# Kernel tuning notes

Measured on AMD Instinct MI355X. Metric: run time of the kernel, lower is better.

The kernel has to match this reference:

```python
import jax, jax.numpy as jnp
import numpy as np


def setup_inputs() -> dict:
    key = jax.random.key(0)
    k0, k1, k2, k3, k4, k5 = jax.random.split(key, 6)
    L1, L2, B, D = 512, 512, 32, 1024
    inputs1 = jax.random.normal(k0, (L1, B, D), dtype=jnp.float32)
    inputs2 = jax.random.normal(k1, (L2, B, D), dtype=jnp.float32)
    # mask value 0 marks a valid token (module keeps pairs where both masks == 0)
    mask1 = jax.random.randint(k2, (L1, B), 0, 2, dtype=jnp.int64)
    mask2 = jax.random.randint(k3, (L2, B), 0, 2, dtype=jnp.int64)
    W = jax.random.normal(k4, (D, D), dtype=jnp.float32) * 0.02
    b = jax.random.normal(k5, (1,), dtype=jnp.float32) * 0.02
    return {"inputs1": inputs1, "inputs2": inputs2, "mask1": mask1,
            "mask2": mask2, "W": W, "b": b, "k": 256}


def reference(inputs1, inputs2, mask1, mask2, W, b, k):
    # inputs: [len, bsz, hdim]; masks: [len, bsz]
    H1 = jnp.transpose(inputs1, (1, 0, 2))  # [B, L1, D]
    H2 = jnp.transpose(inputs2, (1, 0, 2))  # [B, L2, D]
    # bilinear scores: H1 @ W @ H2^T + b, then relu  -> [B, L1, L2]
    S = jax.nn.relu(jnp.einsum('bid,de,bje->bij', H1, W, H2) + b[0])
    # pair is valid iff both mask entries are 0
    valid = (mask1.T[:, :, None] == 0) & (mask2.T[:, None, :] == 0)  # [B, L1, L2]
    B = S.shape[0]
    S_flat = jnp.where(valid.reshape(B, -1), S.reshape(B, -1), -jnp.inf)
    num_elems = S_flat.shape[1]
    k_actual = min(k, num_elems)
    q, _ = jax.lax.top_k(S_flat, k_actual)  # [B, k_actual]
    # replace -inf tail entries with the last finite value in each row
    neg = jnp.isneginf(q)
    q_num_finite = k_actual - neg.sum(axis=-1)  # [B]
    fill = jnp.take_along_axis(q, (q_num_finite - 1)[:, None], axis=1)  # [B, 1]
    q = jnp.where(neg, fill, q)
    if k_actual < k:
        q = jnp.concatenate(
            [q, jnp.broadcast_to(q[:, -1:], (B, k - k_actual))], axis=1)
    return q
```

## Files before the change

kernel.cpp:

```cpp
#include <hip/hip_runtime.h>

typedef __bf16 bf16_t;
typedef bf16_t bf16x8 __attribute__((ext_vector_type(8)));
typedef float floatx4 __attribute__((ext_vector_type(4)));

#define L1C 512
#define L2C 512
#define BC  32
#define DC  1024
#define KTOP 256
#define NBIN 4096
#define CAP  512
#define NT   64
#define FBUF 16384

__device__ __forceinline__ unsigned short f2bf(float f) {
    unsigned u = __float_as_uint(f);
    u += 0x7FFFu + ((u >> 16) & 1u);
    return (unsigned short)(u >> 16);
}

__device__ __forceinline__ void g2l16(const unsigned short* g, unsigned short* l) {
    __builtin_amdgcn_global_load_lds((const unsigned int*)g, (unsigned int*)l,
                                     16, 0, 0);
}

__device__ __forceinline__ float decode_key(unsigned k) {
    return __uint_as_float(k & 0x7FFFFFFFu);
}

__global__ __launch_bounds__(512) void scan_kernel(
    const int* __restrict__ mask1, const int* __restrict__ mask2,
    int* __restrict__ idx1, int* __restrict__ idx2,
    unsigned* __restrict__ nv1, unsigned* __restrict__ nv2,
    unsigned* __restrict__ cnt) {
    __shared__ unsigned sc[512];
    int b = blockIdx.x, t = threadIdx.x;
    for (int which = 0; which < 2; which++) {
        const int* m = which ? mask2 : mask1;
        int* idx = which ? idx2 : idx1;
        unsigned v = (m[t * BC + b] == 0) ? 1u : 0u;
        sc[t] = v;
        __syncthreads();
        for (int off = 1; off < 512; off <<= 1) {
            unsigned x = (t >= off) ? sc[t - off] : 0u;
            __syncthreads();
            sc[t] += x;
            __syncthreads();
        }
        if (v) idx[b * 512 + sc[t] - 1] = t;
        if (t == 511) { if (which) nv2[b] = sc[511]; else nv1[b] = sc[511]; }
        __syncthreads();
    }
    if (t < NT) cnt[b * NT + t] = 0;
}

__global__ __launch_bounds__(256) void prep_kernel(
    const float* __restrict__ in1, const float* __restrict__ in2,
    const float* __restrict__ W,
    const int* __restrict__ idx1, const int* __restrict__ idx2,
    const unsigned* __restrict__ nv1, const unsigned* __restrict__ nv2,
    unsigned short* __restrict__ A1c, unsigned short* __restrict__ A2c,
    unsigned short* __restrict__ Wb) {
    int r = blockIdx.x, t = threadIdx.x;
    const float* src;
    unsigned short* dst;
    if (r < 2 * 16384) {
        int which = r >> 14;
        int rr = r & 16383;
        int b = rr >> 9, vi = rr & 511;
        unsigned nv = which ? nv2[b] : nv1[b];
        unsigned pad = (nv + 63u) & ~63u;
        if ((unsigned)vi >= pad) return;
        dst = (which ? A2c : A1c) + ((size_t)b * 512 + vi) * DC;
        if ((unsigned)vi < nv) {
            int l = (which ? idx2 : idx1)[b * 512 + vi];
            src = (which ? in2 : in1) + (size_t)(l * BC + b) * DC;
        } else {
            ushort4 z = {0, 0, 0, 0};
            reinterpret_cast<ushort4*>(dst)[t] = z;
            return;
        }
    } else {
        int r3 = r - 2 * 16384;
        src = W + (size_t)r3 * DC;
        dst = Wb + (size_t)r3 * DC;
    }
    float4 v = reinterpret_cast<const float4*>(src)[t];
    ushort4 o;
    o.x = f2bf(v.x); o.y = f2bf(v.y); o.z = f2bf(v.z); o.w = f2bf(v.w);
    reinterpret_cast<ushort4*>(dst)[t] = o;
}

__global__ __launch_bounds__(256) void gemm1_kernel(
    const unsigned short* __restrict__ A,
    const unsigned short* __restrict__ Bt,
    unsigned short* __restrict__ C,
    const unsigned* __restrict__ nv2) {
    int bi = blockIdx.x >> 2, mt = blockIdx.x & 3;
    unsigned pad2 = (nv2[bi] + 63u) & ~63u;
    if ((unsigned)(mt * 128) >= pad2) return;
    __shared__ unsigned short As[2][128][32];
    __shared__ unsigned short Bs[2][128][32];
    int tid = threadIdx.x;
    int wave = tid >> 6, lane = tid & 63;
    int lane15 = lane & 15, quad = lane >> 4;
    int wm = wave >> 1, wn = wave & 1;
    size_t m0 = (size_t)bi * 512 + mt * 128;
    size_t n0 = (size_t)blockIdx.y * 128;

    floatx4 zero = {0.f, 0.f, 0.f, 0.f};
    floatx4 acc[4][4];
#pragma unroll
    for (int i = 0; i < 4; i++)
#pragma unroll
        for (int j = 0; j < 4; j++) acc[i][j] = zero;

    for (int k0 = 0; k0 < DC; k0 += 64) {
#pragma unroll
        for (int c = 0; c < 4; c++) {
            int cid = c * 256 + tid;
            int h = cid >> 9, row = (cid >> 2) & 127, col8 = (cid & 3) * 8;
            unsigned short* lb = &As[0][0][0] + (c * 256 + wave * 64) * 8;
            g2l16(&A[(m0 + row) * DC + k0 + h * 32 + col8], lb);
            unsigned short* lb2 = &Bs[0][0][0] + (c * 256 + wave * 64) * 8;
            g2l16(&Bt[(n0 + row) * DC + k0 + h * 32 + col8], lb2);
        }
        __syncthreads();
#pragma unroll
        for (int h = 0; h < 2; h++) {
            bf16x8 af[4], bfr[4];
#pragma unroll
            for (int mi = 0; mi < 4; mi++)
                af[mi] = *reinterpret_cast<const bf16x8*>(
                    &As[h][wm * 64 + mi * 16 + lane15][quad * 8]);
#pragma unroll
            for (int ni = 0; ni < 4; ni++)
                bfr[ni] = *reinterpret_cast<const bf16x8*>(
                    &Bs[h][wn * 64 + ni * 16 + lane15][quad * 8]);
#pragma unroll
            for (int mi = 0; mi < 4; mi++)
#pragma unroll
                for (int ni = 0; ni < 4; ni++)
                    acc[mi][ni] = __builtin_amdgcn_mfma_f32_16x16x32_bf16(
                        af[mi], bfr[ni], acc[mi][ni], 0, 0, 0);
        }
        __syncthreads();
    }
#pragma unroll
    for (int mi = 0; mi < 4; mi++)
#pragma unroll
        for (int ni = 0; ni < 4; ni++)
#pragma unroll
            for (int r = 0; r < 4; r++) {
                size_t row = m0 + wm * 64 + mi * 16 + quad * 4 + r;
                size_t col = n0 + wn * 64 + ni * 16 + lane15;
                C[row * DC + col] = f2bf(acc[mi][ni][r]);
            }
}

__global__ __launch_bounds__(256) void gemm2_kernel(
    const unsigned short* __restrict__ A1c,
    const unsigned short* __restrict__ V,
    const unsigned* __restrict__ nv1, const unsigned* __restrict__ nv2,
    const float* __restrict__ bptr,
    unsigned* __restrict__ cand,
    unsigned* __restrict__ cnt) {
    int L = blockIdx.x;
    int xcd = L & 7, tile = (L >> 3) & 63, chunk = L >> 9;
    int b = xcd + (chunk << 3);
    int tx = tile & 7, ty = tile >> 3;
    int m0 = ty * 64, n0 = tx * 64;
    int gblk = b * NT + tile;
    int tid = threadIdx.x;
    unsigned nv1v = nv1[b], nv2v = nv2[b];
    unsigned pad1 = (nv1v + 63u) & ~63u, pad2 = (nv2v + 63u) & ~63u;
    if ((unsigned)m0 >= pad1 || (unsigned)n0 >= pad2) {
        if (tid == 0) cnt[gblk] = 0;
        return;
    }
    __shared__ unsigned short As[2][64][32];
    __shared__ unsigned short Bs[2][64][32];
    __shared__ unsigned lh[NBIN];
    __shared__ unsigned csum[256];
    __shared__ unsigned sel_c, sel_a, tsh, lcnt, zeq;
    int wave = tid >> 6, lane = tid & 63;
    int lane15 = lane & 15, quad = lane >> 4;
    const unsigned short* Ab = A1c + (size_t)b * 512 * DC;
    const unsigned short* Bb = V + (size_t)b * 512 * DC;

    for (int i = tid; i < NBIN; i += 256) lh[i] = 0;
    if (tid == 0) { sel_c = 0xFFFFFFFFu; lcnt = 0; zeq = 0; }

    floatx4 zero = {0.f, 0.f, 0.f, 0.f};
    floatx4 acc[4];
#pragma unroll
    for (int i = 0; i < 4; i++) acc[i] = zero;

    for (int k0 = 0; k0 < DC; k0 += 64) {
#pragma unroll
        for (int c = 0; c < 2; c++) {
            int cid = c * 256 + tid;
            int h = cid >> 8, row = (cid >> 2) & 63, col8 = (cid & 3) * 8;
            unsigned short* lb = &As[0][0][0] + (c * 256 + wave * 64) * 8;
            g2l16(&Ab[(size_t)(m0 + row) * DC + k0 + h * 32 + col8], lb);
            unsigned short* lb2 = &Bs[0][0][0] + (c * 256 + wave * 64) * 8;
            g2l16(&Bb[(size_t)(n0 + row) * DC + k0 + h * 32 + col8], lb2);
        }
        __syncthreads();
#pragma unroll
        for (int h = 0; h < 2; h++) {
            bf16x8 af, bfr[4];
            af = *reinterpret_cast<const bf16x8*>(
                &As[h][wave * 16 + lane15][quad * 8]);
#pragma unroll
            for (int ni = 0; ni < 4; ni++)
                bfr[ni] = *reinterpret_cast<const bf16x8*>(
                    &Bs[h][ni * 16 + lane15][quad * 8]);
#pragma unroll
            for (int ni = 0; ni < 4; ni++)
                acc[ni] = __builtin_amdgcn_mfma_f32_16x16x32_bf16(
                    af, bfr[ni], acc[ni], 0, 0, 0);
        }
        __syncthreads();
    }

    float bias = bptr[0];
    unsigned zc = 0;
#pragma unroll
    for (int ni = 0; ni < 4; ni++) {
        int jl = n0 + ni * 16 + lane15;
        int v2 = (unsigned)jl < nv2v;
#pragma unroll
        for (int r = 0; r < 4; r++) {
            int il = m0 + wave * 16 + quad * 4 + r;
            float s = acc[ni][r] + bias;
            if (v2 && (unsigned)il < nv1v) {
                if (s > 0.f)
                    atomicAdd(&lh[(__float_as_uint(s) | 0x80000000u) >> 20], 1u);
                else
                    zc++;
            }
        }
    }
    if (zc) atomicAdd(&lh[2048], zc);
    __syncthreads();
    unsigned s16 = 0;
#pragma unroll
    for (int i = 0; i < 16; i++) s16 += lh[tid * 16 + i];
    csum[tid] = s16;
    __syncthreads();
    for (int off = 1; off < 256; off <<= 1) {
        unsigned v = (tid + off < 256) ? csum[tid + off] : 0u;
        __syncthreads();
        csum[tid] += v;
        __syncthreads();
    }
    {
        unsigned above = (tid < 255) ? csum[tid + 1] : 0u;
        if (tid >= 128 && csum[tid] >= KTOP && above < KTOP) {
            sel_c = (unsigned)tid; sel_a = above;
        }
    }
    __syncthreads();
    if (tid == 0) {
        if (sel_c == 0xFFFFFFFFu) {
            tsh = 2048u << 20;
        } else {
            unsigned cum = sel_a, bin = 2048;
            for (int bb = (int)sel_c * 16 + 15; bb >= (int)sel_c * 16; --bb) {
                unsigned hb = lh[bb];
                if (cum + hb >= KTOP) { bin = (unsigned)bb; break; }
                cum += hb;
            }
            tsh = bin << 20;
        }
    }
    __syncthreads();
    unsigned T = tsh;
    unsigned base = (unsigned)gblk * CAP;
#pragma unroll
    for (int ni = 0; ni < 4; ni++) {
        int jl = n0 + ni * 16 + lane15;
        int v2 = (unsigned)jl < nv2v;
#pragma unroll
        for (int r = 0; r < 4; r++) {
            int il = m0 + wave * 16 + quad * 4 + r;
            float s = acc[ni][r] + bias;
            s = s > 0.f ? s : 0.f;
            unsigned key = (v2 && (unsigned)il < nv1v)
                               ? (__float_as_uint(s) | 0x80000000u) : 0u;
            if (key > T) {
                unsigned p = atomicAdd(&lcnt, 1u);
                if (p < CAP) cand[base + p] = key;
            } else if (key == T) {
                unsigned z = atomicAdd(&zeq, 1u);
                if (z < KTOP) {
                    unsigned p = atomicAdd(&lcnt, 1u);
                    if (p < CAP) cand[base + p] = key;
                }
            }
        }
    }
    __syncthreads();
    if (tid == 0) cnt[gblk] = lcnt < CAP ? lcnt : CAP;
}

__global__ __launch_bounds__(1024) void final_kernel(
    const unsigned* __restrict__ cand, const unsigned* __restrict__ cnt,
    float* __restrict__ out) {
    __shared__ unsigned buf[FBUF];
    __shared__ unsigned h[NBIN];
    __shared__ unsigned ss[256];
    __shared__ unsigned scnt_s[NT], off_s[NT];
    __shared__ unsigned ntot_s, sel_c, sel_a, B_s, R_s, mcount;
    __shared__ int have_s;
    __shared__ unsigned srt[256];
    int b = blockIdx.x, tid = threadIdx.x;
    int wv = tid >> 6, ln = tid & 63;

    if (tid < NT) {
        unsigned c = cnt[b * NT + tid];
        scnt_s[tid] = c < CAP ? c : CAP;
    }
    __syncthreads();
    if (tid == 0) {
        unsigned o = 0;
        for (int i = 0; i < NT; i++) {
            unsigned c = scnt_s[i];
            if (o + c > FBUF) c = (o < FBUF) ? FBUF - o : 0;
            scnt_s[i] = c;
            off_s[i] = o;
            o += c;
        }
        ntot_s = o;
        have_s = 1;
    }
    __syncthreads();
    for (int s = wv; s < NT; s += 16) {
        unsigned c = scnt_s[s], o = off_s[s];
        const unsigned* p = cand + (size_t)(b * NT + s) * CAP;
        for (unsigned i = ln; i < c; i += 64) buf[o + i] = p[i];
    }
    __syncthreads();
    unsigned n = ntot_s;

    unsigned Kr = KTOP;
    unsigned pfx = 0;
    unsigned kth = 0;
    for (int pass = 0; pass < 3; pass++) {
        int bins = (pass < 2) ? NBIN : 256;
        int shift = (pass == 0) ? 20 : (pass == 1) ? 8 : 0;
        int nch = bins >> 4;
        for (int i = tid; i < bins; i += 1024) h[i] = 0;
        __syncthreads();
        for (unsigned i = tid; i < n; i += 1024) {
            unsigned k = buf[i];
            bool ok = (pass == 0) ||
                      (pass == 1 && (k >> 20) == pfx) ||
                      (pass == 2 && (k >> 8) == pfx);
            if (ok) atomicAdd(&h[(k >> shift) & (bins - 1)], 1u);
        }
        __syncthreads();
        if (tid < nch) {
            unsigned s = 0;
#pragma unroll
            for (int i = 0; i < 16; i++) s += h[tid * 16 + i];
            ss[tid] = s;
        }
        __syncthreads();
        for (int off = 1; off < nch; off <<= 1) {
            unsigned v = 0;
            if (tid < nch && tid + (unsigned)off < (unsigned)nch) v = ss[tid + off];
            __syncthreads();
            if (tid < nch) ss[tid] += v;
            __syncthreads();
        }
        if (pass == 0) {
            if (tid == 0) have_s = (ss[0] >= KTOP);
            __syncthreads();
            if (!have_s) break;
        }
        if (tid < nch) {
            unsigned above = (tid + 1 < (unsigned)nch) ? ss[tid + 1] : 0u;
            if (above < Kr && ss[tid] >= Kr) { sel_c = tid; sel_a = above; }
        }
        __syncthreads();
        if (tid == 0) {
            unsigned cum = sel_a;
            for (int bb = (int)sel_c * 16 + 15; bb >= (int)sel_c * 16; --bb) {
                unsigned hb = h[bb];
                if (cum + hb >= Kr) { B_s = (unsigned)bb; R_s = Kr - cum; break; }
                cum += hb;
            }
        }
        __syncthreads();
        unsigned Bv = B_s;
        Kr = R_s;
        if (pass == 0) pfx = Bv;
        else if (pass == 1) pfx = (pfx << 12) | Bv;
        else kth = (pfx << 8) | Bv;
        __syncthreads();
    }

    if (tid == 0) mcount = 0;
    __syncthreads();
    int have = have_s;
    unsigned lim = have ? kth : 0u;
    for (unsigned i = tid; i < n; i += 1024) {
        unsigned k = buf[i];
        if (k > lim) {
            unsigned p = atomicAdd(&mcount, 1u);
            if (p < 256) srt[p] = k;
        }
    }
    __syncthreads();
    unsigned m = mcount;
    if (tid < 256 && tid >= (int)m) srt[tid] = have ? kth : 0u;
    for (int k2 = 2; k2 <= 256; k2 <<= 1) {
        for (int j2 = k2 >> 1; j2 > 0; j2 >>= 1) {
            __syncthreads();
            if (tid < 256) {
                int ixj = tid ^ j2;
                if (ixj > tid) {
                    unsigned a = srt[tid], c = srt[ixj];
                    bool up = (tid & k2) == 0;
                    if (up ? (a < c) : (a > c)) { srt[tid] = c; srt[ixj] = a; }
                }
            }
        }
    }
    __syncthreads();
    if (tid < 256) {
        unsigned nval = have ? KTOP : (m < KTOP ? m : KTOP);
        float v;
        if ((unsigned)tid < nval) v = decode_key(srt[tid]);
        else v = (nval > 0) ? decode_key(srt[nval - 1]) : -__builtin_inff();
        out[b * KTOP + tid] = v;
    }
}

extern "C" void kernel_launch(void* const* d_in, const int* in_sizes, int n_in,
                              void* d_out, int out_size, void* d_ws, size_t ws_size,
                              hipStream_t stream) {
    const float* in1   = (const float*)d_in[0];
    const float* in2   = (const float*)d_in[1];
    const int*   mask1 = (const int*)d_in[2];
    const int*   mask2 = (const int*)d_in[3];
    const float* W     = (const float*)d_in[4];
    const float* bias  = (const float*)d_in[5];
    float* out = (float*)d_out;

    char* ws = (char*)d_ws;
    size_t off = 0;
    const size_t nElem = (size_t)512 * BC * DC;
    unsigned short* A1c = (unsigned short*)(ws + off); off += nElem * 2;
    unsigned short* A2c = (unsigned short*)(ws + off); off += nElem * 2;
    unsigned short* Wb  = (unsigned short*)(ws + off); off += (size_t)DC * DC * 2;
    unsigned short* V   = (unsigned short*)(ws + off); off += nElem * 2;
    unsigned* cand = (unsigned*)(ws + off); off += (size_t)BC * NT * CAP * 4;
    unsigned* cnt  = (unsigned*)(ws + off); off += (size_t)BC * NT * 4;
    int* idx1 = (int*)(ws + off); off += (size_t)BC * 512 * 4;
    int* idx2 = (int*)(ws + off); off += (size_t)BC * 512 * 4;
    unsigned* nv1 = (unsigned*)(ws + off); off += BC * 4;
    unsigned* nv2 = (unsigned*)(ws + off); off += BC * 4;

    scan_kernel<<<BC, 512, 0, stream>>>(mask1, mask2, idx1, idx2, nv1, nv2, cnt);
    prep_kernel<<<2 * 16384 + 1024, 256, 0, stream>>>(
        in1, in2, W, idx1, idx2, nv1, nv2, A1c, A2c, Wb);
    gemm1_kernel<<<dim3(128, 8), 256, 0, stream>>>(A2c, Wb, V, nv2);
    gemm2_kernel<<<2048, 256, 0, stream>>>(A1c, V, nv1, nv2, bias, cand, cnt);
    final_kernel<<<BC, 1024, 0, stream>>>(cand, cnt, out);
}
```

Baseline: 248.2 us.

## Double-buffer LDS tiles in both GEMMs and shrink gemm1 M-tile

Both GEMM kernels now keep two LDS buffers. The loads for the next 64-wide K slice are issued before the MFMA work on the current slice, so global-to-LDS transfer can overlap compute instead of waiting behind a barrier. gemm1 also changes its block tile from 128x128 to 64x128, with each wave owning a 64x32 strip, and launches twice as many blocks. That gives more parallelism and finer skipping of padded rows, at the cost of more redundant loads of the B operand. Double buffering doubles the GEMM LDS footprint, which may reduce occupancy, especially in gemm2, which also holds a 4096-bin histogram in LDS.

```diff
diff --git a/kernel.cpp b/kernel.cpp
--- a/kernel.cpp
+++ b/kernel.cpp
@@ -97,51 +97,62 @@
     const unsigned short* __restrict__ Bt,
     unsigned short* __restrict__ C,
     const unsigned* __restrict__ nv2) {
-    int bi = blockIdx.x >> 2, mt = blockIdx.x & 3;
+    int bi = blockIdx.x >> 3, mt = blockIdx.x & 7;
     unsigned pad2 = (nv2[bi] + 63u) & ~63u;
-    if ((unsigned)(mt * 128) >= pad2) return;
-    __shared__ unsigned short As[2][128][32];
-    __shared__ unsigned short Bs[2][128][32];
+    if ((unsigned)(mt * 64) >= pad2) return;
+    __shared__ unsigned short As[2][2][64][32];
+    __shared__ unsigned short Bs[2][2][128][32];
     int tid = threadIdx.x;
     int wave = tid >> 6, lane = tid & 63;
     int lane15 = lane & 15, quad = lane >> 4;
-    int wm = wave >> 1, wn = wave & 1;
-    size_t m0 = (size_t)bi * 512 + mt * 128;
+    size_t m0 = (size_t)bi * 512 + mt * 64;
     size_t n0 = (size_t)blockIdx.y * 128;
 
     floatx4 zero = {0.f, 0.f, 0.f, 0.f};
-    floatx4 acc[4][4];
+    floatx4 acc[4][2];
 #pragma unroll
     for (int i = 0; i < 4; i++)
 #pragma unroll
-        for (int j = 0; j < 4; j++) acc[i][j] = zero;
-
-    for (int k0 = 0; k0 < DC; k0 += 64) {
+        for (int j = 0; j < 2; j++) acc[i][j] = zero;
+
+    auto stage = [&](int sb, int k0) {
+#pragma unroll
+        for (int c = 0; c < 2; c++) {
+            int cid = c * 256 + tid;
+            int h = cid >> 8, row = (cid >> 2) & 63, col8 = (cid & 3) * 8;
+            unsigned short* lb = &As[sb][0][0][0] + (c * 256 + wave * 64) * 8;
+            g2l16(&A[(m0 + row) * DC + k0 + h * 32 + col8], lb);
+        }
 #pragma unroll
         for (int c = 0; c < 4; c++) {
             int cid = c * 256 + tid;
             int h = cid >> 9, row = (cid >> 2) & 127, col8 = (cid & 3) * 8;
-            unsigned short* lb = &As[0][0][0] + (c * 256 + wave * 64) * 8;
-            g2l16(&A[(m0 + row) * DC + k0 + h * 32 + col8], lb);
-            unsigned short* lb2 = &Bs[0][0][0] + (c * 256 + wave * 64) * 8;
-            g2l16(&Bt[(n0 + row) * DC + k0 + h * 32 + col8], lb2);
-        }
-        __syncthreads();
+            unsigned short* lb = &Bs[sb][0][0][0] + (c * 256 + wave * 64) * 8;
+            g2l16(&Bt[(n0 + row) * DC + k0 + h * 32 + col8], lb);
+        }
+    };
+
+    stage(0, 0);
+    __syncthreads();
+#pragma unroll
+    for (int t = 0; t < DC / 64; t++) {
+        int buf = t & 1;
+        if (t + 1 < DC / 64) stage(buf ^ 1, (t + 1) * 64);
 #pragma unroll
         for (int h = 0; h < 2; h++) {
-            bf16x8 af[4], bfr[4];
+            bf16x8 af[4], bfr[2];
 #pragma unroll
             for (int mi = 0; mi < 4; mi++)
                 af[mi] = *reinterpret_cast<const bf16x8*>(
-                    &As[h][wm * 64 + mi * 16 + lane15][quad * 8]);
-#pragma unroll
-            for (int ni = 0; ni < 4; ni++)
+                    &As[buf][h][mi * 16 + lane15][quad * 8]);
+#pragma unroll
+            for (int ni = 0; ni < 2; ni++)
                 bfr[ni] = *reinterpret_cast<const bf16x8*>(
-                    &Bs[h][wn * 64 + ni * 16 + lane15][quad * 8]);
+                    &Bs[buf][h][wave * 32 + ni * 16 + lane15][quad * 8]);
 #pragma unroll
             for (int mi = 0; mi < 4; mi++)
 #pragma unroll
-                for (int ni = 0; ni < 4; ni++)
+                for (int ni = 0; ni < 2; ni++)
                     acc[mi][ni] = __builtin_amdgcn_mfma_f32_16x16x32_bf16(
                         af[mi], bfr[ni], acc[mi][ni], 0, 0, 0);
         }
@@ -150,11 +161,11 @@
 #pragma unroll
     for (int mi = 0; mi < 4; mi++)
 #pragma unroll
-        for (int ni = 0; ni < 4; ni++)
+        for (int ni = 0; ni < 2; ni++)
 #pragma unroll
             for (int r = 0; r < 4; r++) {
-                size_t row = m0 + wm * 64 + mi * 16 + quad * 4 + r;
-                size_t col = n0 + wn * 64 + ni * 16 + lane15;
+                size_t row = m0 + mi * 16 + quad * 4 + r;
+                size_t col = n0 + wave * 32 + ni * 16 + lane15;
                 C[row * DC + col] = f2bf(acc[mi][ni][r]);
             }
 }
@@ -179,8 +190,8 @@
         if (tid == 0) cnt[gblk] = 0;
         return;
     }
-    __shared__ unsigned short As[2][64][32];
-    __shared__ unsigned short Bs[2][64][32];
+    __shared__ unsigned short As[2][2][64][32];
+    __shared__ unsigned short Bs[2][2][64][32];
     __shared__ unsigned lh[NBIN];
     __shared__ unsigned csum[256];
     __shared__ unsigned sel_c, sel_a, tsh, lcnt, zeq;
@@ -197,26 +208,33 @@
 #pragma unroll
     for (int i = 0; i < 4; i++) acc[i] = zero;
 
-    for (int k0 = 0; k0 < DC; k0 += 64) {
+    auto stage = [&](int sb, int k0) {
 #pragma unroll
         for (int c = 0; c < 2; c++) {
             int cid = c * 256 + tid;
             int h = cid >> 8, row = (cid >> 2) & 63, col8 = (cid & 3) * 8;
-            unsigned short* lb = &As[0][0][0] + (c * 256 + wave * 64) * 8;
+            unsigned short* lb = &As[sb][0][0][0] + (c * 256 + wave * 64) * 8;
             g2l16(&Ab[(size_t)(m0 + row) * DC + k0 + h * 32 + col8], lb);
-            unsigned short* lb2 = &Bs[0][0][0] + (c * 256 + wave * 64) * 8;
+            unsigned short* lb2 = &Bs[sb][0][0][0] + (c * 256 + wave * 64) * 8;
             g2l16(&Bb[(size_t)(n0 + row) * DC + k0 + h * 32 + col8], lb2);
         }
-        __syncthreads();
+    };
+
+    stage(0, 0);
+    __syncthreads();
+#pragma unroll
+    for (int t = 0; t < DC / 64; t++) {
+        int buf = t & 1;
+        if (t + 1 < DC / 64) stage(buf ^ 1, (t + 1) * 64);
 #pragma unroll
         for (int h = 0; h < 2; h++) {
             bf16x8 af, bfr[4];
             af = *reinterpret_cast<const bf16x8*>(
-                &As[h][wave * 16 + lane15][quad * 8]);
+                &As[buf][h][wave * 16 + lane15][quad * 8]);
 #pragma unroll
             for (int ni = 0; ni < 4; ni++)
                 bfr[ni] = *reinterpret_cast<const bf16x8*>(
-                    &Bs[h][ni * 16 + lane15][quad * 8]);
+                    &Bs[buf][h][ni * 16 + lane15][quad * 8]);
 #pragma unroll
             for (int ni = 0; ni < 4; ni++)
                 acc[ni] = __builtin_amdgcn_mfma_f32_16x16x32_bf16(
@@ -468,7 +486,7 @@
     scan_kernel<<<BC, 512, 0, stream>>>(mask1, mask2, idx1, idx2, nv1, nv2, cnt);
     prep_kernel<<<2 * 16384 + 1024, 256, 0, stream>>>(
         in1, in2, W, idx1, idx2, nv1, nv2, A1c, A2c, Wb);
-    gemm1_kernel<<<dim3(128, 8), 256, 0, stream>>>(A2c, Wb, V, nv2);
+    gemm1_kernel<<<dim3(256, 8), 256, 0, stream>>>(A2c, Wb, V, nv2);
     gemm2_kernel<<<2048, 256, 0, stream>>>(A1c, V, nv1, nv2, bias, cand, cnt);
     final_kernel<<<BC, 1024, 0, stream>>>(cand, cnt, out);
 }
```

Result: slower. 268.2 us (+8.1%).

## Double-buffer LDS tiles in both GEMM kernels with async prefetch of next k-step

Applied to the files above, without the earlier changes.

Both GEMM kernels now keep two LDS buffers and issue the global-to-LDS loads for the next k-step before computing on the current one. Partial s_waitcnt vmcnt counts replace the full __syncthreads, so the next tile's loads can stay in flight while the MFMAs run. The aim is to hide global memory latency behind compute. The cost is doubled LDS use, which may lower occupancy, especially in gemm2 where the histogram also lives in LDS. The correctness of the barriers now depends on hand-written waitcnt counts and compiler fences.

```diff
diff --git a/kernel.cpp b/kernel.cpp
--- a/kernel.cpp
+++ b/kernel.cpp
@@ -28,6 +28,8 @@
 __device__ __forceinline__ float decode_key(unsigned k) {
     return __uint_as_float(k & 0x7FFFFFFFu);
 }
+
+#define CFENCE asm volatile("" ::: "memory")
 
 __global__ __launch_bounds__(512) void scan_kernel(
     const int* __restrict__ mask1, const int* __restrict__ mask2,
@@ -100,8 +102,10 @@
     int bi = blockIdx.x >> 2, mt = blockIdx.x & 3;
     unsigned pad2 = (nv2[bi] + 63u) & ~63u;
     if ((unsigned)(mt * 128) >= pad2) return;
-    __shared__ unsigned short As[2][128][32];
-    __shared__ unsigned short Bs[2][128][32];
+    __shared__ unsigned short As0[2][128][32];
+    __shared__ unsigned short Bs0[2][128][32];
+    __shared__ unsigned short As1[2][128][32];
+    __shared__ unsigned short Bs1[2][128][32];
     int tid = threadIdx.x;
     int wave = tid >> 6, lane = tid & 63;
     int lane15 = lane & 15, quad = lane >> 4;
@@ -116,28 +120,49 @@
 #pragma unroll
         for (int j = 0; j < 4; j++) acc[i][j] = zero;
 
-    for (int k0 = 0; k0 < DC; k0 += 64) {
+    auto stage = [&](unsigned short* la, unsigned short* lb, int k0) {
 #pragma unroll
         for (int c = 0; c < 4; c++) {
             int cid = c * 256 + tid;
             int h = cid >> 9, row = (cid >> 2) & 127, col8 = (cid & 3) * 8;
-            unsigned short* lb = &As[0][0][0] + (c * 256 + wave * 64) * 8;
-            g2l16(&A[(m0 + row) * DC + k0 + h * 32 + col8], lb);
-            unsigned short* lb2 = &Bs[0][0][0] + (c * 256 + wave * 64) * 8;
-            g2l16(&Bt[(n0 + row) * DC + k0 + h * 32 + col8], lb2);
-        }
-        __syncthreads();
+            g2l16(&A[(m0 + row) * DC + k0 + h * 32 + col8],
+                  la + (c * 256 + wave * 64) * 8);
+        }
+#pragma unroll
+        for (int c = 0; c < 4; c++) {
+            int cid = c * 256 + tid;
+            int h = cid >> 9, row = (cid >> 2) & 127, col8 = (cid & 3) * 8;
+            g2l16(&Bt[(n0 + row) * DC + k0 + h * 32 + col8],
+                  lb + (c * 256 + wave * 64) * 8);
+        }
+    };
+
+    stage(&As0[0][0][0], &Bs0[0][0][0], 0);
+#pragma unroll
+    for (int t = 0; t < DC / 64; t++) {
+        const unsigned short* curA = (t & 1) ? &As1[0][0][0] : &As0[0][0][0];
+        const unsigned short* curB = (t & 1) ? &Bs1[0][0][0] : &Bs0[0][0][0];
+        if (t + 1 < DC / 64) {
+            unsigned short* nxtA = (t & 1) ? &As0[0][0][0] : &As1[0][0][0];
+            unsigned short* nxtB = (t & 1) ? &Bs0[0][0][0] : &Bs1[0][0][0];
+            stage(nxtA, nxtB, (t + 1) * 64);
+            asm volatile("s_waitcnt vmcnt(8)" ::: "memory");
+        } else {
+            asm volatile("s_waitcnt vmcnt(0)" ::: "memory");
+        }
+        __builtin_amdgcn_s_barrier();
+        CFENCE;
 #pragma unroll
         for (int h = 0; h < 2; h++) {
             bf16x8 af[4], bfr[4];
 #pragma unroll
             for (int mi = 0; mi < 4; mi++)
                 af[mi] = *reinterpret_cast<const bf16x8*>(
-                    &As[h][wm * 64 + mi * 16 + lane15][quad * 8]);
+                    curA + h * 4096 + (wm * 64 + mi * 16 + lane15) * 32 + quad * 8);
 #pragma unroll
             for (int ni = 0; ni < 4; ni++)
                 bfr[ni] = *reinterpret_cast<const bf16x8*>(
-                    &Bs[h][wn * 64 + ni * 16 + lane15][quad * 8]);
+                    curB + h * 4096 + (wn * 64 + ni * 16 + lane15) * 32 + quad * 8);
 #pragma unroll
             for (int mi = 0; mi < 4; mi++)
 #pragma unroll
@@ -145,7 +170,11 @@
                     acc[mi][ni] = __builtin_amdgcn_mfma_f32_16x16x32_bf16(
                         af[mi], bfr[ni], acc[mi][ni], 0, 0, 0);
         }
-        __syncthreads();
+        if (t + 1 < DC / 64) {
+            CFENCE;
+            __builtin_amdgcn_s_barrier();
+            CFENCE;
+        }
     }
 #pragma unroll
     for (int mi = 0; mi < 4; mi++)
@@ -179,8 +208,10 @@
         if (tid == 0) cnt[gblk] = 0;
         return;
     }
-    __shared__ unsigned short As[2][64][32];
-    __shared__ unsigned short Bs[2][64][32];
+    __shared__ unsigned short As0[2][64][32];
+    __shared__ unsigned short Bs0[2][64][32];
+    __shared__ unsigned short As1[2][64][32];
+    __shared__ unsigned short Bs1[2][64][32];
     __shared__ unsigned lh[NBIN];
     __shared__ unsigned csum[256];
     __shared__ unsigned sel_c, sel_a, tsh, lcnt, zeq;
@@ -197,32 +228,50 @@
 #pragma unroll
     for (int i = 0; i < 4; i++) acc[i] = zero;
 
-    for (int k0 = 0; k0 < DC; k0 += 64) {
+    auto stage = [&](unsigned short* la, unsigned short* lb, int k0) {
 #pragma unroll
         for (int c = 0; c < 2; c++) {
             int cid = c * 256 + tid;
             int h = cid >> 8, row = (cid >> 2) & 63, col8 = (cid & 3) * 8;
-            unsigned short* lb = &As[0][0][0] + (c * 256 + wave * 64) * 8;
-            g2l16(&Ab[(size_t)(m0 + row) * DC + k0 + h * 32 + col8], lb);
-            unsigned short* lb2 = &Bs[0][0][0] + (c * 256 + wave * 64) * 8;
-            g2l16(&Bb[(size_t)(n0 + row) * DC + k0 + h * 32 + col8], lb2);
-        }
-        __syncthreads();
+            g2l16(&Ab[(size_t)(m0 + row) * DC + k0 + h * 32 + col8],
+                  la + (c * 256 + wave * 64) * 8);
+            g2l16(&Bb[(size_t)(n0 + row) * DC + k0 + h * 32 + col8],
+                  lb + (c * 256 + wave * 64) * 8);
+        }
+    };
+
+    stage(&As0[0][0][0], &Bs0[0][0][0], 0);
+#pragma unroll
+    for (int t = 0; t < DC / 64; t++) {
+        const unsigned short* curA = (t & 1) ? &As1[0][0][0] : &As0[0][0][0];
+        const unsigned short* curB = (t & 1) ? &Bs1[0][0][0] : &Bs0[0][0][0];
+        if (t + 1 < DC / 64) {
+            unsigned short* nxtA = (t & 1) ? &As0[0][0][0] : &As1[0][0][0];
+            unsigned short* nxtB = (t & 1) ? &Bs0[0][0][0] : &Bs1[0][0][0];
+            stage(nxtA, nxtB, (t + 1) * 64);
+            asm volatile("s_waitcnt vmcnt(4)" ::: "memory");
+        } else {
+            asm volatile("s_waitcnt vmcnt(0)" ::: "memory");
+        }
+        __builtin_amdgcn_s_barrier();
+        CFENCE;
 #pragma unroll
         for (int h = 0; h < 2; h++) {
             bf16x8 af, bfr[4];
             af = *reinterpret_cast<const bf16x8*>(
-                &As[h][wave * 16 + lane15][quad * 8]);
+                curA + h * 2048 + (wave * 16 + lane15) * 32 + quad * 8);
 #pragma unroll
             for (int ni = 0; ni < 4; ni++)
                 bfr[ni] = *reinterpret_cast<const bf16x8*>(
-                    &Bs[h][ni * 16 + lane15][quad * 8]);
+                    curB + h * 2048 + (ni * 16 + lane15) * 32 + quad * 8);
 #pragma unroll
             for (int ni = 0; ni < 4; ni++)
                 acc[ni] = __builtin_amdgcn_mfma_f32_16x16x32_bf16(
                     af, bfr[ni], acc[ni], 0, 0, 0);
         }
-        __syncthreads();
+        CFENCE;
+        __builtin_amdgcn_s_barrier();
+        CFENCE;
     }
 
     float bias = bptr[0];
```

After: 246.0 us. No clear change (-0.9%).
